# Kernel optimization log

Measured on AMD Instinct MI355X. Metric: run time of the kernel, lower is better.

## Reference

```python
import jax, jax.numpy as jnp
import numpy as np

N = 50000          # nodes
E = 800000         # edges (avg degree 16)
F_IN = 64          # raw node features
H = 128            # hidden width (n_hidden[0..5])
H6 = 256           # n_hidden[6]
H7 = 128           # n_hidden[7]
EDGE_DIM = 21


def _lin(k, fan_in, fan_out):
    return jax.random.normal(k, (fan_in, fan_out), jnp.float32) * (1.0 / np.sqrt(fan_in))


def setup_inputs() -> dict:
    key = jax.random.key(0)
    ks = jax.random.split(key, 32)
    inp = {
        "G": jax.random.normal(ks[0], (N, F_IN), jnp.float32),
        "edge_index": jax.random.randint(ks[1], (2, E), 0, N, jnp.int32),
        "edge_attr": jax.random.normal(ks[2], (E, EDGE_DIM), jnp.float32),
        # MLP embedding
        "We1": _lin(ks[3], F_IN, H), "be1": jnp.zeros((H,), jnp.float32),
        "We2": _lin(ks[4], H, H),    "be2": jnp.zeros((H,), jnp.float32),
        "We3": _lin(ks[5], H, H),    "be3": jnp.zeros((H,), jnp.float32),
        # conv1 (ResGatedGraphConv, edge_dim=21)
        "c1_Wk": _lin(ks[6], H, H),  "c1_bk": jnp.zeros((H,), jnp.float32),
        "c1_Wq": _lin(ks[7], H, H),  "c1_bq": jnp.zeros((H,), jnp.float32),
        "c1_Wv": _lin(ks[8], H, H),  "c1_bv": jnp.zeros((H,), jnp.float32),
        "c1_We": _lin(ks[9], EDGE_DIM, H),
        "c1_Ws": _lin(ks[10], H, H), "c1_bs": jnp.zeros((H,), jnp.float32),
        # conv2
        "c2_Wk": _lin(ks[11], H, H), "c2_bk": jnp.zeros((H,), jnp.float32),
        "c2_Wq": _lin(ks[12], H, H), "c2_bq": jnp.zeros((H,), jnp.float32),
        "c2_Wv": _lin(ks[13], H, H), "c2_bv": jnp.zeros((H,), jnp.float32),
        "c2_We": _lin(ks[14], EDGE_DIM, H),
        "c2_Ws": _lin(ks[15], H, H), "c2_bs": jnp.zeros((H,), jnp.float32),
        # graph-level MLP
        "Wg1": _lin(ks[16], H, H),   "bg1": jnp.zeros((H,), jnp.float32),
        "Wg2": _lin(ks[17], H, H),   "bg2": jnp.zeros((H,), jnp.float32),
        # head (input is concat(node_emb, graph_mean) -> 2*H)
        "Wl1": _lin(ks[18], 2 * H, H6), "bl1": jnp.zeros((H6,), jnp.float32),
        "Wl2": _lin(ks[19], H6, H7),    "bl2": jnp.zeros((H7,), jnp.float32),
        "Wl3": _lin(ks[20], H7, 1),     "bl3": jnp.zeros((1,), jnp.float32),
    }
    return inp


def _res_gated_conv(x, src, dst, ea, Wk, bk, Wq, bq, Wv, bv, We, Ws, bs):
    """PyG ResGatedGraphConv with edge_dim:
    msg = sigmoid((k_i + e) + (q_j + e)) * (v_j + e), scatter-add to target i."""
    k = x @ Wk + bk            # [N,H] keys (target side)
    q = x @ Wq + bq            # [N,H] queries (source side)
    v = x @ Wv + bv            # [N,H] values (source side)
    e = ea @ We                # [E,H] edge transform (no bias)
    gate = jax.nn.sigmoid(k[dst] + q[src] + 2.0 * e)   # [E,H]
    msg = gate * (v[src] + e)                           # [E,H]
    agg = jax.ops.segment_sum(msg, dst, num_segments=x.shape[0])
    return agg + x @ Ws + bs   # root/skip connection


def reference(G, edge_index, edge_attr,
              We1, be1, We2, be2, We3, be3,
              c1_Wk, c1_bk, c1_Wq, c1_bq, c1_Wv, c1_bv, c1_We, c1_Ws, c1_bs,
              c2_Wk, c2_bk, c2_Wq, c2_bq, c2_Wv, c2_bv, c2_We, c2_Ws, c2_bs,
              Wg1, bg1, Wg2, bg2,
              Wl1, bl1, Wl2, bl2, Wl3, bl3):
    src, dst = edge_index[0], edge_index[1]
    h = jax.nn.relu(G @ We1 + be1)
    h = jax.nn.relu(h @ We2 + be2)
    h = jax.nn.relu(h @ We3 + be3)
    h = jax.nn.relu(_res_gated_conv(h, src, dst, edge_attr,
                                    c1_Wk, c1_bk, c1_Wq, c1_bq, c1_Wv, c1_bv,
                                    c1_We, c1_Ws, c1_bs))
    h = jax.nn.relu(_res_gated_conv(h, src, dst, edge_attr,
                                    c2_Wk, c2_bk, c2_Wq, c2_bq, c2_Wv, c2_bv,
                                    c2_We, c2_Ws, c2_bs))
    h = jax.nn.relu(h @ Wg1 + bg1)
    h = h @ Wg2 + bg2                      # [N,H]
    gmean = jnp.mean(h, axis=0)            # graph embedding [H]
    u = jnp.concatenate([h, jnp.broadcast_to(gmean, h.shape)], axis=-1)  # [N,2H]
    u = jax.nn.relu(u @ Wl1 + bl1)
    u = jax.nn.relu(u @ Wl2 + bl2)
    u = (u @ Wl3 + bl3).squeeze(-1)        # [N] per-node scalar logits
    return u
```

## Files before the change

kernel.cpp:

```cpp
#include <hip/hip_runtime.h>
#include <hip/hip_fp16.h>

#define NN 50000
#define NE 800000
#define HH 128
#define SCAN_BS 512
#define SCAN_NB 98
#define LDK 40
#define LDA 136
#define LDU 264
#define EBLK ((NE + 255) / 256)

typedef _Float16 half8 __attribute__((ext_vector_type(8)));
typedef float f32x4  __attribute__((ext_vector_type(4)));

__global__ __launch_bounds__(256)
void prep_kernel(const float* __restrict__ s0,  const float* __restrict__ s1,
                 const float* __restrict__ s2,  const float* __restrict__ s3,
                 const float* __restrict__ s4,  const float* __restrict__ s5,
                 const float* __restrict__ s6,  const float* __restrict__ s7,
                 const float* __restrict__ s8,  const float* __restrict__ s9,
                 const float* __restrict__ s10, const float* __restrict__ s11,
                 const float* __restrict__ s12, const float* __restrict__ s13,
                 const float* __restrict__ s14, _Float16* __restrict__ wps,
                 const int* __restrict__ ei, int* __restrict__ deg)
{
    const int b = blockIdx.x;
    if (b >= 480) {
        const int e = (b - 480) * 256 + threadIdx.x;
        if (e < NE) atomicAdd(&deg[ei[NE + e]], 1);
        return;
    }
    const float* srcs[15] = {s0,s1,s2,s3,s4,s5,s6,s7,s8,s9,s10,s11,s12,s13,s14};
    const int Ks[15]   = {64,128,128,128,128,128,128,128,128,128,128,128,128,128,256};
    const int logKs[15]= { 6,  7,  7,  7,  7,  7,  7,  7,  7,  7,  7,  7,  7,  7,  8};
    const int off[15]  = {0,8192,24576,40960,57344,73728,90112,106496,122880,
                          139264,155648,172032,188416,204800,237568};

    const int mi = b >> 5;
    const int bx = b & 31;
    const float* src = srcs[mi];
    const int K = Ks[mi], logK = logKs[mi];
    const int N = (mi == 13) ? 256 : 128;
    _Float16* dst = wps + off[mi];
    const int tot = K * N;
    const int base = (bx * 256 + threadIdx.x) * 4;
    if (base >= tot) return;
    const int n = base >> logK;
    const int k = base & (K - 1);
#pragma unroll
    for (int x = 0; x < 4; ++x)
        dst[(size_t)n * K + k + x] = (_Float16)src[(size_t)(k + x) * N + n];
}

template<bool RELU>
__device__ __forceinline__ void layer_l2l(
    const _Float16* __restrict__ actA, int lda, int K,
    const _Float16* __restrict__ Bt,
    const float* __restrict__ bias,
    _Float16* __restrict__ actO, int ldo, int oc0,
    _Float16* __restrict__ Bs)
{
    const int t = threadIdx.x, lane = t & 63;
    const int wr = (t >> 6) >> 1, wc = (t >> 6) & 1;
    const int fr = lane & 15, fg = lane >> 4;
    const int rb = t >> 1, kb = (t & 1) * 16;

    f32x4 acc[2][4] = {};
    for (int k0 = 0; k0 < K; k0 += 32) {
        const _Float16* p = Bt + (size_t)rb * K + k0 + kb;
        const half8 v0 = *reinterpret_cast<const half8*>(p);
        const half8 v1 = *reinterpret_cast<const half8*>(p + 8);
        *reinterpret_cast<half8*>(&Bs[rb * LDK + kb])     = v0;
        *reinterpret_cast<half8*>(&Bs[rb * LDK + kb + 8]) = v1;
        __syncthreads();

        half8 a[2], bfr[4];
#pragma unroll
        for (int i = 0; i < 2; ++i)
            a[i] = *reinterpret_cast<const half8*>(&actA[(wr * 32 + i * 16 + fr) * lda + k0 + fg * 8]);
#pragma unroll
        for (int j = 0; j < 4; ++j)
            bfr[j] = *reinterpret_cast<const half8*>(&Bs[(wc * 64 + j * 16 + fr) * LDK + fg * 8]);
#pragma unroll
        for (int i = 0; i < 2; ++i)
#pragma unroll
            for (int j = 0; j < 4; ++j)
                acc[i][j] = __builtin_amdgcn_mfma_f32_16x16x32_f16(a[i], bfr[j], acc[i][j], 0, 0, 0);
        __syncthreads();
    }
#pragma unroll
    for (int j = 0; j < 4; ++j) {
        const int gnl = wc * 64 + j * 16 + fr;
        const float bv = bias[gnl];
#pragma unroll
        for (int i = 0; i < 2; ++i)
#pragma unroll
            for (int rr = 0; rr < 4; ++rr) {
                float v = acc[i][j][rr] + bv;
                if (RELU) v = fmaxf(v, 0.f);
                actO[(wr * 32 + i * 16 + fg * 4 + rr) * ldo + oc0 + gnl] = (_Float16)v;
            }
    }
    __syncthreads();
}

__global__ __launch_bounds__(256)
void phase5_kernel(const int* __restrict__ ei, const int* __restrict__ offs,
                   int* __restrict__ cur, const float* __restrict__ ea,
                   int* __restrict__ csr_src, unsigned* __restrict__ ea2,
                   const float* __restrict__ G,
                   const _Float16* __restrict__ W1, const float* __restrict__ b1,
                   const _Float16* __restrict__ W2, const float* __restrict__ b2,
                   const _Float16* __restrict__ W3, const float* __restrict__ b3,
                   _Float16* __restrict__ outf, int M)
{
    __shared__ __attribute__((aligned(16))) _Float16 AA[64 * LDA];
    __shared__ __attribute__((aligned(16))) _Float16 AB[64 * LDA];
    __shared__ __attribute__((aligned(16))) _Float16 Bs[128 * LDK];

    const int t = threadIdx.x;
    if (blockIdx.x < EBLK) {
        const int e = blockIdx.x * 256 + t;
        if (e >= NE) return;
        const int d = ei[NE + e];
        const int p = offs[d] + atomicAdd(&cur[d], 1);
        csr_src[p] = ei[e];
        const float* src = ea + (size_t)e * 21;
        unsigned* dst = ea2 + (size_t)p * 21;
#pragma unroll
        for (int q = 0; q < 21; ++q) {
            const __half2 h = __floats2half2_rn(src[q], src[q]);
            dst[q] = __builtin_bit_cast(unsigned, h);
        }
        return;
    }

    const int m0 = (blockIdx.x - EBLK) << 6;
    {
        const int r  = t >> 2;
        const int c0 = (t & 3) * 16;
        const int gm = m0 + r;
#pragma unroll
        for (int h = 0; h < 2; ++h) {
            float4 v0 = make_float4(0.f, 0.f, 0.f, 0.f), v1 = v0;
            if (gm < M) {
                v0 = *reinterpret_cast<const float4*>(G + (size_t)gm * 64 + c0 + h * 8);
                v1 = *reinterpret_cast<const float4*>(G + (size_t)gm * 64 + c0 + h * 8 + 4);
            }
            half8 hv;
            hv[0] = (_Float16)v0.x; hv[1] = (_Float16)v0.y;
            hv[2] = (_Float16)v0.z; hv[3] = (_Float16)v0.w;
            hv[4] = (_Float16)v1.x; hv[5] = (_Float16)v1.y;
            hv[6] = (_Float16)v1.z; hv[7] = (_Float16)v1.w;
            *reinterpret_cast<half8*>(&AA[r * LDA + c0 + h * 8]) = hv;
        }
    }
    __syncthreads();

    layer_l2l<true>(AA, LDA, 64,  W1, b1, AB, LDA, 0, Bs);
    layer_l2l<true>(AB, LDA, 128, W2, b2, AA, LDA, 0, Bs);
    layer_l2l<true>(AA, LDA, 128, W3, b3, AB, LDA, 0, Bs);

    {
        const int r  = t >> 2;
        const int c0 = (t & 3) * 32;
        const int gm = m0 + r;
        if (gm < M) {
#pragma unroll
            for (int x = 0; x < 32; x += 8)
                *reinterpret_cast<half8*>(outf + (size_t)gm * 128 + c0 + x) =
                    *reinterpret_cast<const half8*>(&AB[r * LDA + c0 + x]);
        }
    }
}

__global__ __launch_bounds__(256)
void kqvs_kernel(const _Float16* __restrict__ act,
                 const _Float16* __restrict__ B0, const _Float16* __restrict__ B1,
                 const _Float16* __restrict__ B2, const _Float16* __restrict__ B3,
                 const float* __restrict__ b0, const float* __restrict__ b1,
                 const float* __restrict__ b2, const float* __restrict__ b3,
                 _Float16* __restrict__ ksb, _Float16* __restrict__ qvb, int M)
{
    __shared__ __attribute__((aligned(16))) _Float16 AA[64 * LDA];
    __shared__ __attribute__((aligned(16))) _Float16 Bs[128 * LDK];

    const int t  = threadIdx.x, lane = t & 63;
    const int m0 = blockIdx.x << 6;
    const int wr = (t >> 6) >> 1, wc = (t >> 6) & 1;
    const int fr = lane & 15, fg = lane >> 4;
    const int rb = t >> 1, kb = (t & 1) * 16;

    {
        const int r  = t >> 2;
        const int c0 = (t & 3) * 32;
        const int gm = m0 + r;
#pragma unroll
        for (int x = 0; x < 32; x += 8) {
            half8 v = {0,0,0,0,0,0,0,0};
            if (gm < M) v = *reinterpret_cast<const half8*>(act + (size_t)gm * 128 + c0 + x);
            *reinterpret_cast<half8*>(&AA[r * LDA + c0 + x]) = v;
        }
    }
    __syncthreads();

#pragma unroll
    for (int nb = 0; nb < 4; ++nb) {
        const _Float16* Bt = (nb == 0) ? B0 : (nb == 1) ? B1 : (nb == 2) ? B2 : B3;
        const float*    bt = (nb == 0) ? b0 : (nb == 1) ? b1 : (nb == 2) ? b2 : b3;
        _Float16* dst = (nb < 2) ? ksb : qvb;
        const int sub = (nb & 1) * 2;
        const float scl = (nb == 0 || nb == 2) ? -1.44269504f : 1.0f;

        f32x4 acc[2][4] = {};
        for (int k0 = 0; k0 < 128; k0 += 32) {
            const _Float16* p = Bt + (size_t)rb * 128 + k0 + kb;
            const half8 v0 = *reinterpret_cast<const half8*>(p);
            const half8 v1 = *reinterpret_cast<const half8*>(p + 8);
            *reinterpret_cast<half8*>(&Bs[rb * LDK + kb])     = v0;
            *reinterpret_cast<half8*>(&Bs[rb * LDK + kb + 8]) = v1;
            __syncthreads();

            half8 a[2], b[4];
#pragma unroll
            for (int i = 0; i < 2; ++i)
                a[i] = *reinterpret_cast<const half8*>(&AA[(wr * 32 + i * 16 + fr) * LDA + k0 + fg * 8]);
#pragma unroll
            for (int j = 0; j < 4; ++j)
                b[j] = *reinterpret_cast<const half8*>(&Bs[(wc * 64 + j * 16 + fr) * LDK + fg * 8]);
#pragma unroll
            for (int i = 0; i < 2; ++i)
#pragma unroll
                for (int j = 0; j < 4; ++j)
                    acc[i][j] = __builtin_amdgcn_mfma_f32_16x16x32_f16(a[i], b[j], acc[i][j], 0, 0, 0);
            __syncthreads();
        }
#pragma unroll
        for (int j = 0; j < 4; ++j) {
            const int gnl = wc * 64 + j * 16 + fr;
            const int pos = ((gnl >> 1) << 2) + sub + (gnl & 1);
            const float bv = bt[gnl];
#pragma unroll
            for (int i = 0; i < 2; ++i) {
                const int mbase = m0 + wr * 32 + i * 16 + fg * 4;
#pragma unroll
                for (int rr = 0; rr < 4; ++rr) {
                    const int gm = mbase + rr;
                    if (gm < M)
                        dst[(size_t)gm * 256 + pos] = (_Float16)((acc[i][j][rr] + bv) * scl);
                }
            }
        }
    }
}

__global__ __launch_bounds__(256)
void graph2_kernel(const _Float16* __restrict__ act,
                   const _Float16* __restrict__ Wg1t, const float* __restrict__ bg1,
                   const _Float16* __restrict__ Wg2t, const float* __restrict__ bg2,
                   _Float16* __restrict__ g2f, float* __restrict__ gsum, int M)
{
    __shared__ __attribute__((aligned(16))) _Float16 AA[64 * LDA];
    __shared__ __attribute__((aligned(16))) _Float16 AB[64 * LDA];
    __shared__ __attribute__((aligned(16))) _Float16 Bs[128 * LDK];

    const int t  = threadIdx.x, lane = t & 63;
    const int m0 = blockIdx.x << 6;
    const int wr = (t >> 6) >> 1, wc = (t >> 6) & 1;
    const int fr = lane & 15, fg = lane >> 4;
    const int rb = t >> 1, kb = (t & 1) * 16;

    {
        const int r  = t >> 2;
        const int c0 = (t & 3) * 32;
        const int gm = m0 + r;
#pragma unroll
        for (int x = 0; x < 32; x += 8) {
            half8 v = {0,0,0,0,0,0,0,0};
            if (gm < M) v = *reinterpret_cast<const half8*>(act + (size_t)gm * 128 + c0 + x);
            *reinterpret_cast<half8*>(&AA[r * LDA + c0 + x]) = v;
        }
    }
    __syncthreads();

    layer_l2l<true>(AA, LDA, 128, Wg1t, bg1, AB, LDA, 0, Bs);

    f32x4 acc[2][4] = {};
    for (int k0 = 0; k0 < 128; k0 += 32) {
        const _Float16* p = Wg2t + (size_t)rb * 128 + k0 + kb;
        const half8 v0 = *reinterpret_cast<const half8*>(p);
        const half8 v1 = *reinterpret_cast<const half8*>(p + 8);
        *reinterpret_cast<half8*>(&Bs[rb * LDK + kb])     = v0;
        *reinterpret_cast<half8*>(&Bs[rb * LDK + kb + 8]) = v1;
        __syncthreads();
        half8 a[2], b[4];
#pragma unroll
        for (int i = 0; i < 2; ++i)
            a[i] = *reinterpret_cast<const half8*>(&AB[(wr * 32 + i * 16 + fr) * LDA + k0 + fg * 8]);
#pragma unroll
        for (int j = 0; j < 4; ++j)
            b[j] = *reinterpret_cast<const half8*>(&Bs[(wc * 64 + j * 16 + fr) * LDK + fg * 8]);
#pragma unroll
        for (int i = 0; i < 2; ++i)
#pragma unroll
            for (int j = 0; j < 4; ++j)
                acc[i][j] = __builtin_amdgcn_mfma_f32_16x16x32_f16(a[i], b[j], acc[i][j], 0, 0, 0);
        __syncthreads();
    }
#pragma unroll
    for (int j = 0; j < 4; ++j) {
        const int gn = wc * 64 + j * 16 + fr;
        const float bv = bg2[gn];
        float csum = 0.f;
#pragma unroll
        for (int i = 0; i < 2; ++i) {
            const int mbase = m0 + wr * 32 + i * 16 + fg * 4;
#pragma unroll
            for (int rr = 0; rr < 4; ++rr) {
                const int gm = mbase + rr;
                if (gm < M) {
                    const float v = acc[i][j][rr] + bv;
                    csum += v;
                    g2f[(size_t)gm * 128 + gn] = (_Float16)v;
                }
            }
        }
        csum += __shfl_xor(csum, 16);
        csum += __shfl_xor(csum, 32);
        if (fg == 0) atomicAdd(&gsum[gn], csum);
    }
}

__global__ __launch_bounds__(256)
void head3_kernel(const _Float16* __restrict__ g2f,
                  const _Float16* __restrict__ Wl1t,
                  const float* __restrict__ gvec,
                  const _Float16* __restrict__ Wl2t,
                  const float* __restrict__ bl2,
                  const float* __restrict__ wl3,
                  const float* __restrict__ bl3,
                  float* __restrict__ out, int M)
{
    __shared__ __attribute__((aligned(16))) _Float16 AA[64 * LDA];
    __shared__ __attribute__((aligned(16))) _Float16 UB[64 * LDU];
    __shared__ __attribute__((aligned(16))) _Float16 Bs[128 * LDK];
    __shared__ float psum[2][64];

    const int t  = threadIdx.x, lane = t & 63;
    const int m0 = blockIdx.x << 6;
    const int wr = (t >> 6) >> 1, wc = (t >> 6) & 1;
    const int fr = lane & 15, fg = lane >> 4;
    const int rb = t >> 1, kb = (t & 1) * 16;

    {
        const int r  = t >> 2;
        const int c0 = (t & 3) * 32;
        const int gm = m0 + r;
#pragma unroll
        for (int x = 0; x < 32; x += 8) {
            half8 v = {0,0,0,0,0,0,0,0};
            if (gm < M) v = *reinterpret_cast<const half8*>(g2f + (size_t)gm * 128 + c0 + x);
            *reinterpret_cast<half8*>(&AA[r * LDA + c0 + x]) = v;
        }
    }
    __syncthreads();

    layer_l2l<true>(AA, LDA, 128, Wl1t,             gvec,       UB, LDU, 0,   Bs);
    layer_l2l<true>(AA, LDA, 128, Wl1t + 128 * 128, gvec + 128, UB, LDU, 128, Bs);

    f32x4 acc[2][4] = {};
    for (int k0 = 0; k0 < 256; k0 += 32) {
        const _Float16* p = Wl2t + (size_t)rb * 256 + k0 + kb;
        const half8 v0 = *reinterpret_cast<const half8*>(p);
        const half8 v1 = *reinterpret_cast<const half8*>(p + 8);
        *reinterpret_cast<half8*>(&Bs[rb * LDK + kb])     = v0;
        *reinterpret_cast<half8*>(&Bs[rb * LDK + kb + 8]) = v1;
        __syncthreads();
        half8 a[2], b[4];
#pragma unroll
        for (int i = 0; i < 2; ++i)
            a[i] = *reinterpret_cast<const half8*>(&UB[(wr * 32 + i * 16 + fr) * LDU + k0 + fg * 8]);
#pragma unroll
        for (int j = 0; j < 4; ++j)
            b[j] = *reinterpret_cast<const half8*>(&Bs[(wc * 64 + j * 16 + fr) * LDK + fg * 8]);
#pragma unroll
        for (int i = 0; i < 2; ++i)
#pragma unroll
            for (int j = 0; j < 4; ++j)
                acc[i][j] = __builtin_amdgcn_mfma_f32_16x16x32_f16(a[i], b[j], acc[i][j], 0, 0, 0);
        __syncthreads();
    }

    float p[2][4] = {};
#pragma unroll
    for (int j = 0; j < 4; ++j) {
        const int gnl = wc * 64 + j * 16 + fr;
        const float bv = bl2[gnl];
        const float wv = wl3[gnl];
#pragma unroll
        for (int i = 0; i < 2; ++i)
#pragma unroll
            for (int rr = 0; rr < 4; ++rr)
                p[i][rr] += fmaxf(acc[i][j][rr] + bv, 0.f) * wv;
    }
#pragma unroll
    for (int i = 0; i < 2; ++i)
#pragma unroll
        for (int rr = 0; rr < 4; ++rr) {
            float s = p[i][rr];
            s += __shfl_xor(s, 1);
            s += __shfl_xor(s, 2);
            s += __shfl_xor(s, 4);
            s += __shfl_xor(s, 8);
            p[i][rr] = s;
        }
    if (fr == 0) {
#pragma unroll
        for (int i = 0; i < 2; ++i)
#pragma unroll
            for (int rr = 0; rr < 4; ++rr)
                psum[wc][wr * 32 + i * 16 + fg * 4 + rr] = p[i][rr];
    }
    __syncthreads();
    if (t < 64) {
        const int gm = m0 + t;
        if (gm < M) out[gm] = psum[0][t] + psum[1][t] + bl3[0];
    }
}

__global__ __launch_bounds__(SCAN_BS)
void scan1_kernel(const int* __restrict__ deg, int* __restrict__ incl,
                  int* __restrict__ bsum)
{
    __shared__ int sm[SCAN_BS];
    const int t = threadIdx.x;
    const int i = blockIdx.x * SCAN_BS + t;
    sm[t] = (i < NN) ? deg[i] : 0;
    __syncthreads();
    for (int d = 1; d < SCAN_BS; d <<= 1) {
        const int add = (t >= d) ? sm[t - d] : 0;
        __syncthreads();
        sm[t] += add;
        __syncthreads();
    }
    if (i < NN) incl[i] = sm[t];
    if (t == SCAN_BS - 1) bsum[blockIdx.x] = sm[t];
}

__global__ __launch_bounds__(128)
void scan2_kernel(int* __restrict__ bsum)
{
    __shared__ int sm[128];
    const int t = threadIdx.x;
    const int v = (t < SCAN_NB) ? bsum[t] : 0;
    sm[t] = v;
    __syncthreads();
    for (int d = 1; d < 128; d <<= 1) {
        const int add = (t >= d) ? sm[t - d] : 0;
        __syncthreads();
        sm[t] += add;
        __syncthreads();
    }
    if (t < SCAN_NB) bsum[t] = sm[t] - v;
}

__global__ __launch_bounds__(SCAN_BS)
void scan3_kernel(const int* __restrict__ incl, const int* __restrict__ deg,
                  const int* __restrict__ bsum, int* __restrict__ offs)
{
    const int t = threadIdx.x;
    const int i = blockIdx.x * SCAN_BS + t;
    if (i < NN) offs[i] = incl[i] - deg[i] + bsum[blockIdx.x];
    if (i == 0) offs[NN] = NE;
}

__global__ __launch_bounds__(256, 8)
void conv_agg_kernel(const int* __restrict__ offs,
                     const int* __restrict__ csr_src,
                     const unsigned* __restrict__ ea2,
                     const float* __restrict__ We,
                     const _Float16* __restrict__ ksb,
                     const _Float16* __restrict__ qvb,
                     _Float16* __restrict__ outh)
{
    const int t    = threadIdx.x;
    const int lane = t & 63;
    const int n    = blockIdx.x * 4 + (t >> 6);
    if (n >= NN) return;

    __half2 w2[21];
#pragma unroll
    for (int q = 0; q < 21; ++q) {
        const float2 wq = *reinterpret_cast<const float2*>(&We[q * HH + 2 * lane]);
        w2[q] = __floats2half2_rn(wq.x, wq.y);
    }

    const uint2 ks = *reinterpret_cast<const uint2*>(ksb + (size_t)n * 256 + lane * 4);
    const __half2 k2 = __builtin_bit_cast(__half2, ks.x);
    const __half2 s2 = __builtin_bit_cast(__half2, ks.y);
    const __half2 one2 = __float2half2_rn(1.f);
    const __half2 cm2  = __float2half2_rn(-2.88539008f);

    const int j0 = __builtin_amdgcn_readfirstlane(offs[n]);
    const int j1 = __builtin_amdgcn_readfirstlane(offs[n + 1]);
    float acc0 = 0.f, acc1 = 0.f;

#define GATHER(S) (*reinterpret_cast<const uint2*>(qvb + (size_t)(S) * 256 + lane * 4))

#define EDGE(QV, J) { \
    const __half2* aa_ = reinterpret_cast<const __half2*>(ea2 + (size_t)(J) * 21); \
    __half2 e01_ = __float2half2_rn(0.f); \
    _Pragma("unroll") \
    for (int q_ = 0; q_ < 21; ++q_) e01_ = __hfma2(aa_[q_], w2[q_], e01_); \
    const __half2 q2_ = __builtin_bit_cast(__half2, (QV).x); \
    const __half2 v2_ = __builtin_bit_cast(__half2, (QV).y); \
    const __half2 arg_ = __hadd2(k2, __hfma2(cm2, e01_, q2_)); \
    const __half2 gate_ = h2rcp(__hadd2(one2, h2exp2(arg_))); \
    const __half2 m_ = __hmul2(gate_, __hadd2(v2_, e01_)); \
    acc0 += __low2float(m_); \
    acc1 += __high2float(m_); }

    int j = j0;
    for (; j + 4 <= j1; j += 4) {
        const int sa = csr_src[j],     sb = csr_src[j + 1];
        const int sc = csr_src[j + 2], sd = csr_src[j + 3];
        const uint2 qva = GATHER(sa);
        const uint2 qvb_ = GATHER(sb);
        const uint2 qvc = GATHER(sc);
        const uint2 qvd = GATHER(sd);
        EDGE(qva, j)
        EDGE(qvb_, j + 1)
        EDGE(qvc, j + 2)
        EDGE(qvd, j + 3)
    }
    for (; j < j1; ++j) {
        const int s_ = csr_src[j];
        const uint2 qv = GATHER(s_);
        EDGE(qv, j)
    }
#undef GATHER
#undef EDGE

    const float r0 = fmaxf(acc0 + __low2float(s2), 0.f);
    const float r1 = fmaxf(acc1 + __high2float(s2), 0.f);
    const __half2 res = __floats2half2_rn(r0, r1);
    *reinterpret_cast<__half2*>(outh + (size_t)n * HH + 2 * lane) = res;
}

__global__ __launch_bounds__(256)
void gvec_kernel(const float* __restrict__ gsum,
                 const float* __restrict__ Wl1,
                 const float* __restrict__ bl1,
                 float* __restrict__ gvec, float invM)
{
    const int j = threadIdx.x;
    float acc = bl1[j];
    for (int k = 0; k < 128; ++k)
        acc += (gsum[k] * invM) * Wl1[(size_t)(128 + k) * 256 + j];
    gvec[j] = acc;
}

extern "C" void kernel_launch(void* const* d_in, const int* in_sizes, int n_in,
                              void* d_out, int out_size, void* d_ws, size_t ws_size,
                              hipStream_t stream)
{
    const float* G   = (const float*)d_in[0];
    const int*   ei  = (const int*)  d_in[1];
    const float* ea  = (const float*)d_in[2];
    const float* We1 = (const float*)d_in[3];  const float* be1 = (const float*)d_in[4];
    const float* We2 = (const float*)d_in[5];  const float* be2 = (const float*)d_in[6];
    const float* We3 = (const float*)d_in[7];  const float* be3 = (const float*)d_in[8];
    const float* c1_Wk = (const float*)d_in[9];  const float* c1_bk = (const float*)d_in[10];
    const float* c1_Wq = (const float*)d_in[11]; const float* c1_bq = (const float*)d_in[12];
    const float* c1_Wv = (const float*)d_in[13]; const float* c1_bv = (const float*)d_in[14];
    const float* c1_We = (const float*)d_in[15];
    const float* c1_Ws = (const float*)d_in[16]; const float* c1_bs = (const float*)d_in[17];
    const float* c2_Wk = (const float*)d_in[18]; const float* c2_bk = (const float*)d_in[19];
    const float* c2_Wq = (const float*)d_in[20]; const float* c2_bq = (const float*)d_in[21];
    const float* c2_Wv = (const float*)d_in[22]; const float* c2_bv = (const float*)d_in[23];
    const float* c2_We = (const float*)d_in[24];
    const float* c2_Ws = (const float*)d_in[25]; const float* c2_bs = (const float*)d_in[26];
    const float* Wg1 = (const float*)d_in[27]; const float* bg1 = (const float*)d_in[28];
    const float* Wg2 = (const float*)d_in[29]; const float* bg2 = (const float*)d_in[30];
    const float* Wl1 = (const float*)d_in[31]; const float* bl1 = (const float*)d_in[32];
    const float* Wl2 = (const float*)d_in[33]; const float* bl2 = (const float*)d_in[34];
    const float* Wl3 = (const float*)d_in[35]; const float* bl3 = (const float*)d_in[36];

    float* out = (float*)d_out;

    char* ws = (char*)d_ws;
    size_t off = 0;
    _Float16* wps  = (_Float16*)(ws + off); off += 270336 * 2;
    _Float16* hA   = (_Float16*)(ws + off); off += (size_t)NN * 128 * 2;
    _Float16* hB   = (_Float16*)(ws + off); off += (size_t)NN * 128 * 2;
    _Float16* ksb  = (_Float16*)(ws + off); off += (size_t)NN * 256 * 2;
    _Float16* qvb  = (_Float16*)(ws + off); off += (size_t)NN * 256 * 2;
    unsigned* ea2  = (unsigned*)(ws + off); off += (size_t)NE * 21 * 4;
    int*      deg  = (int*)     (ws + off); off += (size_t)NN * 4;
    int*      cur  = (int*)     (ws + off); off += (size_t)NN * 4;
    float*    gsum = (float*)   (ws + off); off += 256 * 4;
    float*    gvec = (float*)   (ws + off); off += 256 * 4;
    int*      incl = (int*)     (ws + off); off += (size_t)NN * 4;
    int*      bsum = (int*)     (ws + off); off += 128 * 4;
    int*      offs = (int*)     (ws + off); off += (size_t)(NN + 2) * 4;
    int*      csr_src = (int*)  (ws + off); off += (size_t)NE * 4;

    const int O_We1 = 0,      O_We2 = 8192,   O_We3 = 24576;
    const int O_c1k = 40960,  O_c1s = 57344,  O_c1q = 73728,  O_c1v = 90112;
    const int O_c2k = 106496, O_c2s = 122880, O_c2q = 139264, O_c2v = 155648;
    const int O_Wg1 = 172032, O_Wg2 = 188416, O_Wl1 = 204800, O_Wl2 = 237568;

    const dim3 blk(256);
    const int  MT = (NN + 63) / 64;
    const int  AGGB = (NN + 3) / 4;

    hipMemsetAsync(deg, 0, (size_t)(2 * NN + 256) * 4, stream);
    prep_kernel<<<dim3(480 + EBLK), blk, 0, stream>>>(
        We1, We2, We3, c1_Wk, c1_Ws, c1_Wq, c1_Wv,
        c2_Wk, c2_Ws, c2_Wq, c2_Wv, Wg1, Wg2, Wl1, Wl2, wps, ei, deg);

    scan1_kernel<<<dim3(SCAN_NB), dim3(SCAN_BS), 0, stream>>>(deg, incl, bsum);
    scan2_kernel<<<dim3(1), dim3(128), 0, stream>>>(bsum);
    scan3_kernel<<<dim3(SCAN_NB), dim3(SCAN_BS), 0, stream>>>(incl, deg, bsum, offs);

    phase5_kernel<<<dim3(EBLK + MT), blk, 0, stream>>>(
        ei, offs, cur, ea, csr_src, ea2, G,
        wps + O_We1, be1, wps + O_We2, be2, wps + O_We3, be3, hA, NN);

    kqvs_kernel<<<dim3(MT), blk, 0, stream>>>(hA,
        wps + O_c1k, wps + O_c1s, wps + O_c1q, wps + O_c1v,
        c1_bk, c1_bs, c1_bq, c1_bv, ksb, qvb, NN);
    conv_agg_kernel<<<dim3(AGGB), blk, 0, stream>>>(offs, csr_src, ea2, c1_We,
        ksb, qvb, hB);

    kqvs_kernel<<<dim3(MT), blk, 0, stream>>>(hB,
        wps + O_c2k, wps + O_c2s, wps + O_c2q, wps + O_c2v,
        c2_bk, c2_bs, c2_bq, c2_bv, ksb, qvb, NN);
    conv_agg_kernel<<<dim3(AGGB), blk, 0, stream>>>(offs, csr_src, ea2, c2_We,
        ksb, qvb, hA);

    graph2_kernel<<<dim3(MT), blk, 0, stream>>>(hA,
        wps + O_Wg1, bg1, wps + O_Wg2, bg2, hB, gsum, NN);

    gvec_kernel<<<dim3(1), dim3(256), 0, stream>>>(gsum, Wl1, bl1, gvec, 1.f / NN);

    head3_kernel<<<dim3(MT), blk, 0, stream>>>(hB,
        wps + O_Wl1, gvec, wps + O_Wl2, bl2, Wl3, bl3, out, NN);
}
```

Measured before the change: 454.9 us.

## Merge kqvs weight passes into one 512-thread block and fold tiny kernels via last-block

Restructures the K/Q/V/S projection kernel so one 512-thread block computes all four weight matrices in a single k-loop, staging all weights at once instead of looping four times with repeated barriers. It also removes the scan2 and gvec launches by having the last finishing block of scan1 and graph2 (detected with an atomic counter) do that work. This aims to cut launch overhead and redundant barrier and loop passes. The cost is larger shared memory and register use per block, and a threadfence plus atomic at the end of each block.

```diff
diff --git a/kernel.cpp b/kernel.cpp
--- a/kernel.cpp
+++ b/kernel.cpp
@@ -175,7 +175,7 @@
     }
 }
 
-__global__ __launch_bounds__(256)
+__global__ __launch_bounds__(512)
 void kqvs_kernel(const _Float16* __restrict__ act,
                  const _Float16* __restrict__ B0, const _Float16* __restrict__ B1,
                  const _Float16* __restrict__ B2, const _Float16* __restrict__ B3,
@@ -184,72 +184,79 @@
                  _Float16* __restrict__ ksb, _Float16* __restrict__ qvb, int M)
 {
     __shared__ __attribute__((aligned(16))) _Float16 AA[64 * LDA];
-    __shared__ __attribute__((aligned(16))) _Float16 Bs[128 * LDK];
-
-    const int t  = threadIdx.x, lane = t & 63;
-    const int m0 = blockIdx.x << 6;
-    const int wr = (t >> 6) >> 1, wc = (t >> 6) & 1;
-    const int fr = lane & 15, fg = lane >> 4;
-    const int rb = t >> 1, kb = (t & 1) * 16;
+    __shared__ __attribute__((aligned(16))) _Float16 Bs[512 * LDK];
+
+    const int t    = threadIdx.x, lane = t & 63;
+    const int wid  = t >> 6;
+    const int wr   = wid >> 2;
+    const int wc   = wid & 3;
+    const int fr   = lane & 15, fg = lane >> 4;
+    const int m0   = blockIdx.x << 6;
 
     {
-        const int r  = t >> 2;
-        const int c0 = (t & 3) * 32;
+        const int r  = t >> 3;
+        const int c0 = (t & 7) * 16;
         const int gm = m0 + r;
-#pragma unroll
-        for (int x = 0; x < 32; x += 8) {
-            half8 v = {0,0,0,0,0,0,0,0};
-            if (gm < M) v = *reinterpret_cast<const half8*>(act + (size_t)gm * 128 + c0 + x);
-            *reinterpret_cast<half8*>(&AA[r * LDA + c0 + x]) = v;
-        }
-    }
-    __syncthreads();
-
-#pragma unroll
-    for (int nb = 0; nb < 4; ++nb) {
-        const _Float16* Bt = (nb == 0) ? B0 : (nb == 1) ? B1 : (nb == 2) ? B2 : B3;
-        const float*    bt = (nb == 0) ? b0 : (nb == 1) ? b1 : (nb == 2) ? b2 : b3;
-        _Float16* dst = (nb < 2) ? ksb : qvb;
-        const int sub = (nb & 1) * 2;
-        const float scl = (nb == 0 || nb == 2) ? -1.44269504f : 1.0f;
-
-        f32x4 acc[2][4] = {};
-        for (int k0 = 0; k0 < 128; k0 += 32) {
-            const _Float16* p = Bt + (size_t)rb * 128 + k0 + kb;
-            const half8 v0 = *reinterpret_cast<const half8*>(p);
-            const half8 v1 = *reinterpret_cast<const half8*>(p + 8);
-            *reinterpret_cast<half8*>(&Bs[rb * LDK + kb])     = v0;
-            *reinterpret_cast<half8*>(&Bs[rb * LDK + kb + 8]) = v1;
-            __syncthreads();
-
-            half8 a[2], b[4];
-#pragma unroll
-            for (int i = 0; i < 2; ++i)
-                a[i] = *reinterpret_cast<const half8*>(&AA[(wr * 32 + i * 16 + fr) * LDA + k0 + fg * 8]);
-#pragma unroll
-            for (int j = 0; j < 4; ++j)
-                b[j] = *reinterpret_cast<const half8*>(&Bs[(wc * 64 + j * 16 + fr) * LDK + fg * 8]);
-#pragma unroll
-            for (int i = 0; i < 2; ++i)
-#pragma unroll
-                for (int j = 0; j < 4; ++j)
-                    acc[i][j] = __builtin_amdgcn_mfma_f32_16x16x32_f16(a[i], b[j], acc[i][j], 0, 0, 0);
-            __syncthreads();
-        }
-#pragma unroll
-        for (int j = 0; j < 4; ++j) {
-            const int gnl = wc * 64 + j * 16 + fr;
-            const int pos = ((gnl >> 1) << 2) + sub + (gnl & 1);
-            const float bv = bt[gnl];
-#pragma unroll
-            for (int i = 0; i < 2; ++i) {
-                const int mbase = m0 + wr * 32 + i * 16 + fg * 4;
-#pragma unroll
-                for (int rr = 0; rr < 4; ++rr) {
-                    const int gm = mbase + rr;
-                    if (gm < M)
-                        dst[(size_t)gm * 256 + pos] = (_Float16)((acc[i][j][rr] + bv) * scl);
-                }
+        half8 v0 = {0,0,0,0,0,0,0,0}, v1 = v0;
+        if (gm < M) {
+            v0 = *reinterpret_cast<const half8*>(act + (size_t)gm * 128 + c0);
+            v1 = *reinterpret_cast<const half8*>(act + (size_t)gm * 128 + c0 + 8);
+        }
+        *reinterpret_cast<half8*>(&AA[r * LDA + c0])     = v0;
+        *reinterpret_cast<half8*>(&AA[r * LDA + c0 + 8]) = v1;
+    }
+
+    const _Float16* Bt_stage = (t < 128) ? B0 : (t < 256) ? B1 : (t < 384) ? B2 : B3;
+    const _Float16* srow = Bt_stage + (size_t)(t & 127) * 128;
+
+    __syncthreads();
+
+    f32x4 acc[2][8] = {};
+    for (int k0 = 0; k0 < 128; k0 += 32) {
+        {
+            const half8 v0 = *reinterpret_cast<const half8*>(srow + k0);
+            const half8 v1 = *reinterpret_cast<const half8*>(srow + k0 + 8);
+            const half8 v2 = *reinterpret_cast<const half8*>(srow + k0 + 16);
+            const half8 v3 = *reinterpret_cast<const half8*>(srow + k0 + 24);
+            *reinterpret_cast<half8*>(&Bs[t * LDK + 0])  = v0;
+            *reinterpret_cast<half8*>(&Bs[t * LDK + 8])  = v1;
+            *reinterpret_cast<half8*>(&Bs[t * LDK + 16]) = v2;
+            *reinterpret_cast<half8*>(&Bs[t * LDK + 24]) = v3;
+        }
+        __syncthreads();
+
+        half8 a[2], b[8];
+#pragma unroll
+        for (int i = 0; i < 2; ++i)
+            a[i] = *reinterpret_cast<const half8*>(&AA[(wr * 32 + i * 16 + fr) * LDA + k0 + fg * 8]);
+#pragma unroll
+        for (int j = 0; j < 8; ++j)
+            b[j] = *reinterpret_cast<const half8*>(&Bs[(wc * 128 + j * 16 + fr) * LDK + fg * 8]);
+#pragma unroll
+        for (int i = 0; i < 2; ++i)
+#pragma unroll
+            for (int j = 0; j < 8; ++j)
+                acc[i][j] = __builtin_amdgcn_mfma_f32_16x16x32_f16(a[i], b[j], acc[i][j], 0, 0, 0);
+        __syncthreads();
+    }
+
+    _Float16* dst  = (wc < 2) ? ksb : qvb;
+    const int  sub = (wc & 1) * 2;
+    const float scl = (wc == 0 || wc == 2) ? -1.44269504f : 1.0f;
+    const float* bt = (wc == 0) ? b0 : (wc == 1) ? b1 : (wc == 2) ? b2 : b3;
+#pragma unroll
+    for (int j = 0; j < 8; ++j) {
+        const int gnl = j * 16 + fr;
+        const int pos = ((gnl >> 1) << 2) + sub + (gnl & 1);
+        const float bv = bt[gnl];
+#pragma unroll
+        for (int i = 0; i < 2; ++i) {
+            const int mbase = m0 + wr * 32 + i * 16 + fg * 4;
+#pragma unroll
+            for (int rr = 0; rr < 4; ++rr) {
+                const int gm = mbase + rr;
+                if (gm < M)
+                    dst[(size_t)gm * 256 + pos] = (_Float16)((acc[i][j][rr] + bv) * scl);
             }
         }
     }
@@ -259,7 +266,10 @@
 void graph2_kernel(const _Float16* __restrict__ act,
                    const _Float16* __restrict__ Wg1t, const float* __restrict__ bg1,
                    const _Float16* __restrict__ Wg2t, const float* __restrict__ bg2,
-                   _Float16* __restrict__ g2f, float* __restrict__ gsum, int M)
+                   _Float16* __restrict__ g2f, float* __restrict__ gsum,
+                   const float* __restrict__ Wl1, const float* __restrict__ bl1,
+                   float* __restrict__ gvec, int* __restrict__ cnt,
+                   float invM, int M)
 {
     __shared__ __attribute__((aligned(16))) _Float16 AA[64 * LDA];
     __shared__ __attribute__((aligned(16))) _Float16 AB[64 * LDA];
@@ -329,6 +339,20 @@
         csum += __shfl_xor(csum, 16);
         csum += __shfl_xor(csum, 32);
         if (fg == 0) atomicAdd(&gsum[gn], csum);
+    }
+
+    __shared__ int lastFlag;
+    __shared__ float gs[128];
+    __threadfence();
+    if (t == 0) lastFlag = (atomicAdd(cnt, 1) == (int)gridDim.x - 1) ? 1 : 0;
+    __syncthreads();
+    if (lastFlag) {
+        if (t < 128) gs[t] = atomicAdd(&gsum[t], 0.f) * invM;
+        __syncthreads();
+        float accv = bl1[t];
+        for (int k = 0; k < 128; ++k)
+            accv += gs[k] * Wl1[(size_t)(128 + k) * 256 + t];
+        gvec[t] = accv;
     }
 }
 
@@ -431,7 +455,7 @@
 
 __global__ __launch_bounds__(SCAN_BS)
 void scan1_kernel(const int* __restrict__ deg, int* __restrict__ incl,
-                  int* __restrict__ bsum)
+                  int* __restrict__ bsum, int* __restrict__ cnt)
 {
     __shared__ int sm[SCAN_BS];
     const int t = threadIdx.x;
@@ -446,23 +470,25 @@
     }
     if (i < NN) incl[i] = sm[t];
     if (t == SCAN_BS - 1) bsum[blockIdx.x] = sm[t];
-}
-
-__global__ __launch_bounds__(128)
-void scan2_kernel(int* __restrict__ bsum)
-{
-    __shared__ int sm[128];
-    const int t = threadIdx.x;
-    const int v = (t < SCAN_NB) ? bsum[t] : 0;
-    sm[t] = v;
-    __syncthreads();
-    for (int d = 1; d < 128; d <<= 1) {
-        const int add = (t >= d) ? sm[t - d] : 0;
-        __syncthreads();
-        sm[t] += add;
-        __syncthreads();
-    }
-    if (t < SCAN_NB) bsum[t] = sm[t] - v;
+
+    __shared__ int lastFlag;
+    __shared__ int sb[128];
+    __threadfence();
+    if (t == 0) lastFlag = (atomicAdd(cnt, 1) == (int)gridDim.x - 1) ? 1 : 0;
+    __syncthreads();
+    if (lastFlag) {
+        int v = 0;
+        if (t < SCAN_NB) v = atomicAdd(&bsum[t], 0);
+        if (t < 128) sb[t] = (t < SCAN_NB) ? v : 0;
+        __syncthreads();
+        for (int d = 1; d < 128; d <<= 1) {
+            const int add = (t < 128 && t >= d) ? sb[t - d] : 0;
+            __syncthreads();
+            if (t < 128) sb[t] += add;
+            __syncthreads();
+        }
+        if (t < SCAN_NB) bsum[t] = sb[t] - v;
+    }
 }
 
 __global__ __launch_bounds__(SCAN_BS)
@@ -546,19 +572,6 @@
     const float r1 = fmaxf(acc1 + __high2float(s2), 0.f);
     const __half2 res = __floats2half2_rn(r0, r1);
     *reinterpret_cast<__half2*>(outh + (size_t)n * HH + 2 * lane) = res;
-}
-
-__global__ __launch_bounds__(256)
-void gvec_kernel(const float* __restrict__ gsum,
-                 const float* __restrict__ Wl1,
-                 const float* __restrict__ bl1,
-                 float* __restrict__ gvec, float invM)
-{
-    const int j = threadIdx.x;
-    float acc = bl1[j];
-    for (int k = 0; k < 128; ++k)
-        acc += (gsum[k] * invM) * Wl1[(size_t)(128 + k) * 256 + j];
-    gvec[j] = acc;
 }
 
 extern "C" void kernel_launch(void* const* d_in, const int* in_sizes, int n_in,
@@ -600,6 +613,7 @@
     int*      deg  = (int*)     (ws + off); off += (size_t)NN * 4;
     int*      cur  = (int*)     (ws + off); off += (size_t)NN * 4;
     float*    gsum = (float*)   (ws + off); off += 256 * 4;
+    int*      cnts = (int*)     (ws + off); off += 8 * 4;
     float*    gvec = (float*)   (ws + off); off += 256 * 4;
     int*      incl = (int*)     (ws + off); off += (size_t)NN * 4;
     int*      bsum = (int*)     (ws + off); off += 128 * 4;
@@ -615,35 +629,33 @@
     const int  MT = (NN + 63) / 64;
     const int  AGGB = (NN + 3) / 4;
 
-    hipMemsetAsync(deg, 0, (size_t)(2 * NN + 256) * 4, stream);
+    hipMemsetAsync(deg, 0, (size_t)(2 * NN + 256 + 8) * 4, stream);
     prep_kernel<<<dim3(480 + EBLK), blk, 0, stream>>>(
         We1, We2, We3, c1_Wk, c1_Ws, c1_Wq, c1_Wv,
         c2_Wk, c2_Ws, c2_Wq, c2_Wv, Wg1, Wg2, Wl1, Wl2, wps, ei, deg);
 
-    scan1_kernel<<<dim3(SCAN_NB), dim3(SCAN_BS), 0, stream>>>(deg, incl, bsum);
-    scan2_kernel<<<dim3(1), dim3(128), 0, stream>>>(bsum);
+    scan1_kernel<<<dim3(SCAN_NB), dim3(SCAN_BS), 0, stream>>>(deg, incl, bsum, cnts);
     scan3_kernel<<<dim3(SCAN_NB), dim3(SCAN_BS), 0, stream>>>(incl, deg, bsum, offs);
 
     phase5_kernel<<<dim3(EBLK + MT), blk, 0, stream>>>(
         ei, offs, cur, ea, csr_src, ea2, G,
         wps + O_We1, be1, wps + O_We2, be2, wps + O_We3, be3, hA, NN);
 
-    kqvs_kernel<<<dim3(MT), blk, 0, stream>>>(hA,
+    kqvs_kernel<<<dim3(MT), dim3(512), 0, stream>>>(hA,
         wps + O_c1k, wps + O_c1s, wps + O_c1q, wps + O_c1v,
         c1_bk, c1_bs, c1_bq, c1_bv, ksb, qvb, NN);
     conv_agg_kernel<<<dim3(AGGB), blk, 0, stream>>>(offs, csr_src, ea2, c1_We,
         ksb, qvb, hB);
 
-    kqvs_kernel<<<dim3(MT), blk, 0, stream>>>(hB,
+    kqvs_kernel<<<dim3(MT), dim3(512), 0, stream>>>(hB,
         wps + O_c2k, wps + O_c2s, wps + O_c2q, wps + O_c2v,
         c2_bk, c2_bs, c2_bq, c2_bv, ksb, qvb, NN);
     conv_agg_kernel<<<dim3(AGGB), blk, 0, stream>>>(offs, csr_src, ea2, c2_We,
         ksb, qvb, hA);
 
     graph2_kernel<<<dim3(MT), blk, 0, stream>>>(hA,
-        wps + O_Wg1, bg1, wps + O_Wg2, bg2, hB, gsum, NN);
-
-    gvec_kernel<<<dim3(1), dim3(256), 0, stream>>>(gsum, Wl1, bl1, gvec, 1.f / NN);
+        wps + O_Wg1, bg1, wps + O_Wg2, bg2, hB, gsum,
+        Wl1, bl1, gvec, cnts + 1, 1.f / NN, NN);
 
     head3_kernel<<<dim3(MT), blk, 0, stream>>>(hB,
         wps + O_Wl1, gvec, wps + O_Wl2, bl2, Wl3, bl3, out, NN);
```

Result: slower. 580.4 us (+27.6%).
